# Optimization experiments

Measured on AMD Instinct MI355X. Metric: run time of the kernel, lower is better.

Reference implementation:

```python
import jax, jax.numpy as jnp
import numpy as np
import math

HIDDEN = 2048
NUM_HEADS = 16
NUM_KV_HEADS = 4
HEAD_DIM = 128
GROUPS = NUM_HEADS // NUM_KV_HEADS
BATCH = 1
SEQ = 4096
THETA = 10000.0


def _rope(x):
    # x: [B, h, S, D], interleaved-pair rotation as in the torch module
    seq = x.shape[2]
    freqs = 1.0 / (THETA ** (jnp.arange(0, HEAD_DIM, 2, dtype=jnp.float32) / HEAD_DIM))  # [D/2]
    angles = jnp.arange(seq, dtype=jnp.float32)[:, None] * freqs[None, :]  # [S, D/2]
    cos = jnp.cos(angles)[None, None]  # [1,1,S,D/2]
    sin = jnp.sin(angles)[None, None]
    x1 = x[..., 0::2]
    x2 = x[..., 1::2]
    # stack along new last axis then flatten -> interleaved layout
    rot = jnp.stack([x1 * cos - x2 * sin, x1 * sin + x2 * cos], axis=-1)
    return rot.reshape(x.shape)


def setup_inputs() -> dict:
    key = jax.random.key(0)
    kx, kq, kk, kv, ko = jax.random.split(key, 5)
    scale = 0.02
    x = jax.random.normal(kx, (BATCH, SEQ, HIDDEN), dtype=jnp.float32)
    Wq = jax.random.normal(kq, (NUM_HEADS * HEAD_DIM, HIDDEN), dtype=jnp.float32) * scale
    Wk = jax.random.normal(kk, (NUM_KV_HEADS * HEAD_DIM, HIDDEN), dtype=jnp.float32) * scale
    Wv = jax.random.normal(kv, (NUM_KV_HEADS * HEAD_DIM, HIDDEN), dtype=jnp.float32) * scale
    Wo = jax.random.normal(ko, (HIDDEN, NUM_HEADS * HEAD_DIM), dtype=jnp.float32) * scale
    return {"x": x, "Wq": Wq, "Wk": Wk, "Wv": Wv, "Wo": Wo}


def reference(x, Wq, Wk, Wv, Wo):
    B, S, _ = x.shape
    q = (x @ Wq.T).reshape(B, S, NUM_HEADS, HEAD_DIM).transpose(0, 2, 1, 3)      # [B,16,S,D]
    k = (x @ Wk.T).reshape(B, S, NUM_KV_HEADS, HEAD_DIM).transpose(0, 2, 1, 3)   # [B,4,S,D]
    v = (x @ Wv.T).reshape(B, S, NUM_KV_HEADS, HEAD_DIM).transpose(0, 2, 1, 3)
    q = _rope(q)
    k = _rope(k)
    # GQA: repeat_interleave KV heads across the group dim
    k = jnp.repeat(k, GROUPS, axis=1)  # [B,16,S,D]
    v = jnp.repeat(v, GROUPS, axis=1)
    scale = 1.0 / math.sqrt(HEAD_DIM)
    scores = jnp.einsum("bhqd,bhkd->bhqk", q, k) * scale  # [B,16,S,S]
    causal = jnp.triu(jnp.ones((S, S), dtype=bool), k=1)
    scores = jnp.where(causal[None, None], jnp.float32(-jnp.inf), scores)
    attn = jax.nn.softmax(scores, axis=-1)
    out = jnp.einsum("bhqk,bhkd->bhqd", attn, v)           # [B,16,S,D]
    out = out.transpose(0, 2, 1, 3).reshape(B, S, NUM_HEADS * HEAD_DIM)
    return out @ Wo.T
```

## Files before the change

### kernel.cpp

```cpp
#include <hip/hip_runtime.h>
#include <hip/hip_bf16.h>

typedef unsigned short u16;
typedef unsigned int u32;
typedef short short8 __attribute__((ext_vector_type(8)));
typedef unsigned short ushort4v __attribute__((ext_vector_type(4)));
typedef float f32x4 __attribute__((ext_vector_type(4)));
typedef float f32x16 __attribute__((ext_vector_type(16)));
typedef u32 u32x4 __attribute__((ext_vector_type(4)));

#define SEQN 4096
#define HID 2048
#define NH 16
#define NKV 4
#define HD 128
#define QDIM 2048
#define KVD 512
#define QKVS 3072

static __device__ __forceinline__ float bf2f(u16 u){
  unsigned x = ((unsigned)u) << 16; float f; __builtin_memcpy(&f, &x, 4); return f;
}
static __device__ __forceinline__ u16 f2bf(float f){
  unsigned x; __builtin_memcpy(&x, &f, 4);
  x += 0x7fffu + ((x >> 16) & 1u);
  return (u16)(x >> 16);
}
static __device__ __forceinline__ u16 f2bfc(float f){
  unsigned x; __builtin_memcpy(&x, &f, 4);
  return (u16)((x + 0x8000u) >> 16);
}
static __device__ __forceinline__ u32 pkr(float a, float b){
  u32 ab, bb; __builtin_memcpy(&ab, &a, 4); __builtin_memcpy(&bb, &b, 4);
  return ((ab + 0x8000u) >> 16) | ((bb + 0x8000u) & 0xffff0000u);
}

#define G1 (SEQN*HID/4)
#define G2 (QDIM*HID/4)
#define G3 (KVD*HID/4)
#define G4 (KVD*HID/4)
#define G5 (HID*QDIM/4)
__global__ __launch_bounds__(256) void cvt5_kernel(const float* __restrict__ x,  const float* __restrict__ Wq,
                                                   const float* __restrict__ Wk, const float* __restrict__ Wv,
                                                   const float* __restrict__ Wo, u16* __restrict__ xb,
                                                   u16* __restrict__ Wqkvb, u16* __restrict__ Wob){
  int g = blockIdx.x * 256 + threadIdx.x;
  const float* src; u16* dst; int off;
  if (g < G1)                { src = x;  dst = xb;    off = g; }
  else if (g < G1+G2)        { src = Wq; dst = Wqkvb; off = g - G1; }
  else if (g < G1+G2+G3)     { src = Wk; dst = Wqkvb + (size_t)QDIM*HID;        off = g - (G1+G2); }
  else if (g < G1+G2+G3+G4)  { src = Wv; dst = Wqkvb + (size_t)(QDIM+KVD)*HID;  off = g - (G1+G2+G3); }
  else if (g < G1+G2+G3+G4+G5){ src = Wo; dst = Wob;  off = g - (G1+G2+G3+G4); }
  else return;
  f32x4 v = ((const f32x4*)src)[off];
  ushort4v o;
  o.x = f2bf(v.x); o.y = f2bf(v.y); o.z = f2bf(v.z); o.w = f2bf(v.w);
  ((ushort4v*)dst)[off] = o;
}

#define ROPE_BLKS (SEQN * (NH + NKV) * 16 / 256)
__global__ __launch_bounds__(256) void prep_kernel(u16* __restrict__ QKVb, u16* __restrict__ VTg){
  __shared__ u16 T[64][72];
  const int bid = blockIdx.x;
  const int tid = threadIdx.x;
  if (bid < ROPE_BLKS){
    int idx = bid * 256 + tid;
    int i8 = idx & 15;
    int rest = idx >> 4;
    int h = rest % (NH + NKV);
    int s = rest / (NH + NKV);
    int col = (h < NH) ? h * HD : QDIM + (h - NH) * HD;
    u16* p = QKVb + (size_t)s * QKVS + col + i8 * 8;
    short8 v = *(const short8*)p;
    short8 o;
#pragma unroll
    for (int j = 0; j < 4; j++){
      int i = i8 * 4 + j;
      float freq = expf(-0.14391156831212788f * (float)i);
      float ang = (float)s * freq;
      float c = cosf(ang), sn = sinf(ang);
      float x1 = bf2f((u16)v[2*j]), x2 = bf2f((u16)v[2*j+1]);
      o[2*j]   = (short)f2bfc(x1 * c - x2 * sn);
      o[2*j+1] = (short)f2bfc(x1 * sn + x2 * c);
    }
    *(short8*)p = o;
  } else {
    const int b2 = bid - ROPE_BLKS;
    const int s0 = (b2 & 63) * 64;
    const int c0 = (b2 >> 6) * 64;
    const int sl = tid & 63, ch = tid >> 6;
    const u16* src = QKVb + QDIM + KVD + (size_t)(s0 + sl) * QKVS + c0 + ch * 16;
    *(short8*)&T[sl][ch * 16]     = *(const short8*)(src);
    *(short8*)&T[sl][ch * 16 + 8] = *(const short8*)(src + 8);
    __syncthreads();
#pragma unroll
    for (int it = 0; it < 16; it++){
      int c = it * 4 + ch;
      VTg[(size_t)(c0 + c) * SEQN + s0 + sl] = T[sl][c];
    }
  }
}

static __device__ __forceinline__ void gload16(const void* g, void* l){
  __builtin_amdgcn_global_load_lds((const __attribute__((address_space(1))) void*)g,
                                   (__attribute__((address_space(3))) void*)l, 16, 0, 0);
}

template<int F32OUT>
__global__ __launch_bounds__(256) void gemm_kernel(const u16* __restrict__ A, const u16* __restrict__ B,
                                                   void* __restrict__ Cout, int M, int N, int Kd, int ldc){
  __shared__ alignas(16) u16 sh[32768];
  const int tid = threadIdx.x;
  const int w = tid >> 6, l = tid & 63;
  const int wr = w >> 1, wc = w & 1;
  const int lc = l & 15, lg = l >> 4;
  const int tm = blockIdx.x * 128, tn = blockIdx.y * 128;

  const u16* src[4];
#pragma unroll
  for (int i = 0; i < 4; i++){
    int blk = w * 4 + i;
    int row = (blk & 7) * 16 + (l >> 2);
    int cs  = (l & 3) ^ (row & 3);
    src[i] = (blk < 8) ? (A + (size_t)(tm + row) * Kd + cs * 8)
                       : (B + (size_t)(tn + row) * Kd + cs * 8);
  }

  auto issueStage = [&](int slot, int t){
    char* base = (char*)sh + slot * 16384;
    int k0 = t * 32;
#pragma unroll
    for (int i = 0; i < 4; i++)
      gload16(src[i] + k0, base + (w * 4 + i) * 1024);
  };

  f32x4 acc[4][4] = {};
  const int T = Kd / 32;

  issueStage(0, 0);
  issueStage(1, 1);

  for (int t = 0; t < T; t++){
    if (t + 2 < T) issueStage((t + 2) & 3, t + 2);
    if (t + 2 < T)      asm volatile("s_waitcnt vmcnt(8)" ::: "memory");
    else if (t + 1 < T) asm volatile("s_waitcnt vmcnt(4)" ::: "memory");
    else                asm volatile("s_waitcnt vmcnt(0)" ::: "memory");
    __builtin_amdgcn_s_barrier();
    __builtin_amdgcn_sched_barrier(0);

    const char* base = (const char*)sh + (t & 3) * 16384;
    short8 a[4], b[4];
#pragma unroll
    for (int mi = 0; mi < 4; mi++){
      int row = wr * 64 + mi * 16 + lc;
      a[mi] = *(const short8*)(base + row * 64 + ((lg ^ (row & 3)) * 16));
    }
#pragma unroll
    for (int ni = 0; ni < 4; ni++){
      int row = wc * 64 + ni * 16 + lc;
      b[ni] = *(const short8*)(base + 8192 + row * 64 + ((lg ^ (row & 3)) * 16));
    }
#pragma unroll
    for (int mi = 0; mi < 4; mi++)
#pragma unroll
      for (int ni = 0; ni < 4; ni++)
        acc[mi][ni] = __builtin_amdgcn_mfma_f32_16x16x32_bf16(a[mi], b[ni], acc[mi][ni], 0, 0, 0);
  }

  if (F32OUT){
#pragma unroll
    for (int mi = 0; mi < 4; mi++)
#pragma unroll
      for (int ni = 0; ni < 4; ni++)
#pragma unroll
        for (int r = 0; r < 4; r++){
          int row = tm + wr*64 + mi*16 + lg*4 + r;
          int col = tn + wc*64 + ni*16 + lc;
          ((float*)Cout)[(size_t)row * ldc + col] = acc[mi][ni][r];
        }
  } else {
    __syncthreads();
    u16* Ew = sh + w * 1168;
#pragma unroll
    for (int mi = 0; mi < 4; mi++){
#pragma unroll
      for (int ni = 0; ni < 4; ni++)
#pragma unroll
        for (int r = 0; r < 4; r++)
          Ew[(lg * 4 + r) * 73 + ni * 16 + lc] = f2bfc(acc[mi][ni][r]);
#pragma unroll
      for (int pass = 0; pass < 2; pass++){
        int row = pass * 8 + (l >> 3);
        short8 v;
#pragma unroll
        for (int j = 0; j < 8; j++) v[j] = (short)Ew[row * 73 + (l & 7) * 8 + j];
        *(short8*)((u16*)Cout + (size_t)(tm + wr*64 + mi*16 + row) * ldc + tn + wc*64 + (l & 7) * 8) = v;
      }
    }
  }
}

__global__ __launch_bounds__(256, 2) void attn_kernel(const u16* __restrict__ Qg, const u16* __restrict__ Kgb,
                                                      const u16* __restrict__ VTg, u16* __restrict__ Aout,
                                                      u16* __restrict__ PO, float* __restrict__ mP,
                                                      float* __restrict__ LP){
  __shared__ alignas(16) char pool[65536];

  const int pr  = blockIdx.x;
  const int h   = blockIdx.y;
  const int s   = blockIdx.z;
  const int kvh = h >> 2;
  const int tid = threadIdx.x;
  const int w = tid >> 6, l = tid & 63;
  const int q5 = l & 31;
  const int hi = l >> 5;
  const int hi4 = hi * 4;
  const float csc = 0.12751743f;

  const u16* Ksrc[4];
  const u16* Vsrc[4];
#pragma unroll
  for (int i = 0; i < 4; i++){
    int blk = w * 4 + i;
    int row = blk * 4 + (l >> 4);
    int cg  = (l & 15) ^ (row & 15);
    Ksrc[i] = Kgb + (size_t)row * QKVS + kvh * HD + cg * 8;
    int d   = blk * 8 + (l >> 3);
    int cv  = (l & 7) ^ (d & 7);
    Vsrc[i] = VTg + (size_t)(kvh * 128 + d) * SEQN + cv * 8;
  }

  auto issueTile = [&](int b, int kv0){
    char* Ksb = pool + b * 32768;
    char* VTb = Ksb + 16384;
#pragma unroll
    for (int i = 0; i < 4; i++)
      gload16(Ksrc[i] + (size_t)kv0 * QKVS, Ksb + (w * 4 + i) * 1024);
#pragma unroll
    for (int i = 0; i < 4; i++)
      gload16(Vsrc[i] + kv0, VTb + (w * 4 + i) * 1024);
  };

  const int qlo = pr, qhi = 31 - pr;
  int nseg, sq[2], st0[2], st1[2], smode[2];
  if (s == 0){
    nseg = 2;
    sq[0] = qlo; st0[0] = 0;           st1[0] = 2 * pr + 2;   smode[0] = 0;
    sq[1] = qhi; st0[1] = 0;           st1[1] = 31 - 2 * pr;  smode[1] = 1;
  } else {
    nseg = 1;
    sq[0] = qhi; st0[0] = 31 - 2 * pr; st1[0] = 64 - 2 * pr;  smode[0] = 2;
  }

  for (int sg = 0; sg < nseg; sg++){
    const int qt = sq[sg], t0 = st0[sg], t1 = st1[sg], mode = smode[sg];
    const int qbase = qt * 128 + w * 32;
    const int qa    = qbase + q5;

    short8 qf[8];
    {
      const u16* qp = Qg + (size_t)(qbase + q5) * QKVS + h * HD + hi * 8;
#pragma unroll
      for (int k0 = 0; k0 < 8; k0++) qf[k0] = *(const short8*)(qp + k0 * 16);
    }

    f32x16 Ov[4] = {};
    float Lrow = 0.f;
    float ms = -1e30f;

    auto computeTile = [&](int b, int kv0){
      if (kv0 > qbase + 31) return;
      char* Ksb = pool + b * 32768;
      char* VTb = Ksb + 16384;
      f32x16 Sv[2] = {};
#pragma unroll
      for (int k0 = 0; k0 < 8; k0++){
#pragma unroll
        for (int nb = 0; nb < 2; nb++){
          int kvr = nb * 32 + q5;
          short8 kf = *(const short8*)(Ksb + kvr * 256 + (((k0 * 2 + hi) ^ (kvr & 15)) << 4));
          Sv[nb] = __builtin_amdgcn_mfma_f32_32x32x16_bf16(kf, qf[k0], Sv[nb], 0, 0, 0);
        }
      }
      if (kv0 + 63 > qbase){
#pragma unroll
        for (int nb = 0; nb < 2; nb++)
#pragma unroll
          for (int r = 0; r < 16; r++){
            int kva = kv0 + nb * 32 + (r & 3) + 8 * (r >> 2) + hi4;
            if (kva > qa) Sv[nb][r] = -1e30f;
          }
      }
      float tm = fmaxf(Sv[0][0], Sv[0][1]);
#pragma unroll
      for (int nb = 0; nb < 2; nb++)
#pragma unroll
        for (int r = (nb == 0 ? 2 : 0); r < 16; r += 2)
          tm = fmaxf(tm, fmaxf(Sv[nb][r], Sv[nb][r + 1]));
      tm = fmaxf(tm, __shfl_xor(tm, 32));
      float tms = tm * csc;
      if (!__all(tms - ms <= 8.f)){
        float nms = fmaxf(ms, tms);
        float al = __builtin_amdgcn_exp2f(ms - nms);
        ms = nms;
        Lrow *= al;
#pragma unroll
        for (int nb = 0; nb < 4; nb++)
#pragma unroll
          for (int r = 0; r < 16; r++) Ov[nb][r] *= al;
      }
      float ts0 = 0.f, ts1 = 0.f;
#pragma unroll
      for (int nb = 0; nb < 2; nb++)
#pragma unroll
        for (int r = 0; r < 16; r += 2){
          float p0 = __builtin_amdgcn_exp2f(__builtin_fmaf(Sv[nb][r],     csc, -ms));
          float p1 = __builtin_amdgcn_exp2f(__builtin_fmaf(Sv[nb][r + 1], csc, -ms));
          Sv[nb][r] = p0; Sv[nb][r + 1] = p1;
          ts0 += p0; ts1 += p1;
        }
      float ts = ts0 + ts1;
      ts += __shfl_xor(ts, 32);
      Lrow += ts;
#pragma unroll
      for (int kc = 0; kc < 4; kc++){
        const int nb = kc >> 1, rb = (kc & 1) * 8;
        u32 Aw = pkr(Sv[nb][rb + 0], Sv[nb][rb + 1]);
        u32 Bw = pkr(Sv[nb][rb + 2], Sv[nb][rb + 3]);
        u32 Cw = pkr(Sv[nb][rb + 4], Sv[nb][rb + 5]);
        u32 Dw = pkr(Sv[nb][rb + 6], Sv[nb][rb + 7]);
        u32 sAw = __shfl_xor(Aw, 32);
        u32 sBw = __shfl_xor(Bw, 32);
        u32 sCw = __shfl_xor(Cw, 32);
        u32 sDw = __shfl_xor(Dw, 32);
        u32 w0 = hi ? sCw : Aw;
        u32 w1 = hi ? sDw : Bw;
        u32 w2 = hi ? Cw : sAw;
        u32 w3 = hi ? Dw : sBw;
        u32x4 pw4 = {w0, w1, w2, w3};
        short8 pf = *(short8*)&pw4;
#pragma unroll
        for (int nbd = 0; nbd < 4; nbd++){
          int drow = nbd * 32 + q5;
          short8 vf = *(const short8*)(VTb + drow * 128 + (((kc * 2 + hi) ^ (drow & 7)) << 4));
          Ov[nbd] = __builtin_amdgcn_mfma_f32_32x32x16_bf16(vf, pf, Ov[nbd], 0, 0, 0);
        }
      }
    };

    __syncthreads();
    issueTile(0, t0 * 64);
    __syncthreads();
    int cur = 0;
    for (int t = t0; t < t1; t++){
      if (t + 1 < t1) issueTile(cur ^ 1, (t + 1) * 64);
      computeTile(cur, t * 64);
      __syncthreads();
      cur ^= 1;
    }

    u16* Ew = (u16*)(pool + w * 8704);
    float rl = (mode == 0) ? (1.f / Lrow) : 1.f;
#pragma unroll
    for (int nbd = 0; nbd < 4; nbd++)
#pragma unroll
      for (int r = 0; r < 16; r += 2){
        int d = nbd * 32 + (r & 3) + 8 * (r >> 2) + hi4;
        u32 wpk = pkr(Ov[nbd][r] * rl, Ov[nbd][r + 1] * rl);
        *(u32*)((char*)Ew + q5 * 272 + d * 2) = wpk;
      }
    if (mode == 0){
#pragma unroll
      for (int pass = 0; pass < 8; pass++){
        int q2 = pass * 4 + (l >> 4);
        short8 ov = *(const short8*)((char*)Ew + q2 * 272 + (l & 15) * 16);
        *(short8*)(Aout + (size_t)(qbase + q2) * QDIM + h * HD + (l & 15) * 8) = ov;
      }
    } else {
      const int p = mode - 1;
      u16* dstb = PO + ((size_t)((p * 16 + pr) * NH + h) * 128) * 128;
#pragma unroll
      for (int pass = 0; pass < 8; pass++){
        int q2 = pass * 4 + (l >> 4);
        short8 ov = *(const short8*)((char*)Ew + q2 * 272 + (l & 15) * 16);
        *(short8*)(dstb + (size_t)(w * 32 + q2) * 128 + (l & 15) * 8) = ov;
      }
      if (hi == 0){
        int idx = ((p * 16 + pr) * NH + h) * 128 + w * 32 + q5;
        mP[idx] = ms;
        LP[idx] = Lrow;
      }
    }
  }
}

__global__ __launch_bounds__(256) void combine_kernel(const u16* __restrict__ PO, const float* __restrict__ mP,
                                                      const float* __restrict__ LP, u16* __restrict__ Aout){
  const int pr = blockIdx.x;
  const int h  = blockIdx.y;
  const int tid = threadIdx.x;
  const int r  = tid >> 1;
  const int dh = (tid & 1) * 64;
  const int qhi = 31 - pr;
  const int idx0 = ((0 * 16 + pr) * NH + h) * 128 + r;
  const int idx1 = ((1 * 16 + pr) * NH + h) * 128 + r;
  float m0 = mP[idx0], m1 = mP[idx1];
  float L0 = LP[idx0], L1 = LP[idx1];
  float M = fmaxf(m0, m1);
  float a0 = __builtin_amdgcn_exp2f(m0 - M);
  float a1 = __builtin_amdgcn_exp2f(m1 - M);
  float rl = 1.f / (L0 * a0 + L1 * a1);
  const u16* o0 = PO + (size_t)idx0 * 128 + dh;
  const u16* o1 = PO + (size_t)idx1 * 128 + dh;
  u16* dst = Aout + (size_t)(qhi * 128 + r) * QDIM + h * HD + dh;
#pragma unroll
  for (int ch = 0; ch < 8; ch++){
    short8 v0 = *(const short8*)(o0 + ch * 8);
    short8 v1 = *(const short8*)(o1 + ch * 8);
    u32x4 ow;
#pragma unroll
    for (int j = 0; j < 4; j++){
      float e0 = (bf2f((u16)v0[2*j])   * a0 + bf2f((u16)v1[2*j])   * a1) * rl;
      float e1 = (bf2f((u16)v0[2*j+1]) * a0 + bf2f((u16)v1[2*j+1]) * a1) * rl;
      ow[j] = pkr(e0, e1);
    }
    *(u32x4*)(dst + ch * 8) = ow;
  }
}

extern "C" void kernel_launch(void* const* d_in, const int* in_sizes, int n_in,
                              void* d_out, int out_size, void* d_ws, size_t ws_size,
                              hipStream_t stream){
  const float* x  = (const float*)d_in[0];
  const float* Wq = (const float*)d_in[1];
  const float* Wk = (const float*)d_in[2];
  const float* Wv = (const float*)d_in[3];
  const float* Wo = (const float*)d_in[4];

  char* p = (char*)d_ws;
  u16* xb    = (u16*)p; p += (size_t)SEQN * HID * 2;
  u16* Wqkvb = (u16*)p; p += (size_t)QKVS * HID * 2;
  u16* Wob   = (u16*)p; p += (size_t)HID * QDIM * 2;
  u16* QKVb  = (u16*)p; p += (size_t)SEQN * QKVS * 2;
  u16* Ab    = (u16*)p; p += (size_t)SEQN * QDIM * 2;
  u16* VTg   = (u16*)p; p += (size_t)SEQN * KVD * 2;
  u16* PO    = (u16*)p; p += (size_t)2 * 16 * NH * 128 * 128 * 2;
  float* mP  = (float*)p; p += (size_t)2 * 16 * NH * 128 * 4;
  float* LP  = (float*)p; p += (size_t)2 * 16 * NH * 128 * 4;

  const int totg = G1 + G2 + G3 + G4 + G5;
  cvt5_kernel<<<(totg + 255) / 256, 256, 0, stream>>>(x, Wq, Wk, Wv, Wo, xb, Wqkvb, Wob);

  gemm_kernel<0><<<dim3(SEQN/128, QKVS/128), 256, 0, stream>>>(xb, Wqkvb, QKVb, SEQN, QKVS, HID, QKVS);

  prep_kernel<<<ROPE_BLKS + (SEQN/64) * (KVD/64), 256, 0, stream>>>(QKVb, VTg);

  attn_kernel<<<dim3(16, NH, 2), 256, 0, stream>>>(QKVb, QKVb + QDIM, VTg, Ab, PO, mP, LP);
  combine_kernel<<<dim3(16, NH), 256, 0, stream>>>(PO, mP, LP, Ab);

  gemm_kernel<1><<<dim3(SEQN/128, HID/128), 256, 0, stream>>>(Ab, Wob, d_out, SEQN, HID, QDIM, HID);
}
```

Before: 238.2 us.

## Deepen GEMM pipeline, swizzle block order for XCD locality, raise MFMA priority

The GEMM now uses a five-slot LDS ring with three stages in flight instead of two, adjusting the vmcnt waits to match. It also remaps workgroup IDs so that consecutive tiles land on the same XCD for L2 reuse. The attention kernel remaps its block index so heads sharing a KV head are grouped per XCD, and it wraps its MFMA loops in s_setprio to favour matrix issue. The extra GEMM stage raises LDS use per block, which may lower occupancy. The GEMM swizzle assumes the workgroup count divides evenly by 8.

Result: slower. 245.3 us (+3.0%).

```diff
diff --git a/kernel.cpp b/kernel.cpp
--- a/kernel.cpp
+++ b/kernel.cpp
@@ -109,12 +109,18 @@
 template<int F32OUT>
 __global__ __launch_bounds__(256) void gemm_kernel(const u16* __restrict__ A, const u16* __restrict__ B,
                                                    void* __restrict__ Cout, int M, int N, int Kd, int ldc){
-  __shared__ alignas(16) u16 sh[32768];
+  __shared__ alignas(16) u16 sh[40960];
   const int tid = threadIdx.x;
   const int w = tid >> 6, l = tid & 63;
   const int wr = w >> 1, wc = w & 1;
   const int lc = l & 15, lg = l >> 4;
-  const int tm = blockIdx.x * 128, tn = blockIdx.y * 128;
+
+  const int nbx = gridDim.x;
+  const int nwg = nbx * gridDim.y;
+  const int fid = blockIdx.x + nbx * blockIdx.y;
+  const int cpx = nwg >> 3;
+  const int swz = (fid & 7) * cpx + (fid >> 3);
+  const int tm = (swz % nbx) * 128, tn = (swz / nbx) * 128;
 
   const u16* src[4];
 #pragma unroll
@@ -138,17 +144,21 @@
   const int T = Kd / 32;
 
   issueStage(0, 0);
-  issueStage(1, 1);
-
+  if (1 < T) issueStage(1, 1);
+  if (2 < T) issueStage(2, 2);
+
+  int sw = 3, sr = 0;
   for (int t = 0; t < T; t++){
-    if (t + 2 < T) issueStage((t + 2) & 3, t + 2);
-    if (t + 2 < T)      asm volatile("s_waitcnt vmcnt(8)" ::: "memory");
-    else if (t + 1 < T) asm volatile("s_waitcnt vmcnt(4)" ::: "memory");
-    else                asm volatile("s_waitcnt vmcnt(0)" ::: "memory");
+    if (t + 3 < T){ issueStage(sw, t + 3); if (++sw == 5) sw = 0; }
+    if (t + 3 < T)      asm volatile("s_waitcnt vmcnt(12)" ::: "memory");
+    else if (t + 2 < T) asm volatile("s_waitcnt vmcnt(8)"  ::: "memory");
+    else if (t + 1 < T) asm volatile("s_waitcnt vmcnt(4)"  ::: "memory");
+    else                asm volatile("s_waitcnt vmcnt(0)"  ::: "memory");
     __builtin_amdgcn_s_barrier();
     __builtin_amdgcn_sched_barrier(0);
 
-    const char* base = (const char*)sh + (t & 3) * 16384;
+    const char* base = (const char*)sh + sr * 16384;
+    if (++sr == 5) sr = 0;
     short8 a[4], b[4];
 #pragma unroll
     for (int mi = 0; mi < 4; mi++){
@@ -206,9 +216,12 @@
                                                       float* __restrict__ LP){
   __shared__ alignas(16) char pool[65536];
 
-  const int pr  = blockIdx.x;
-  const int h   = blockIdx.y;
-  const int s   = blockIdx.z;
+  const int fid = blockIdx.x + 16 * (blockIdx.y + NH * blockIdx.z);
+  const int c8  = fid & 7;
+  const int idx = ((c8 & 1) << 6) | (fid >> 3);
+  const int pr  = (idx >> 2) & 15;
+  const int s   = idx >> 6;
+  const int h   = 4 * (c8 >> 1) + (idx & 3);
   const int kvh = h >> 2;
   const int tid = threadIdx.x;
   const int w = tid >> 6, l = tid & 63;
@@ -273,6 +286,7 @@
       char* Ksb = pool + b * 32768;
       char* VTb = Ksb + 16384;
       f32x16 Sv[2] = {};
+      __builtin_amdgcn_s_setprio(1);
 #pragma unroll
       for (int k0 = 0; k0 < 8; k0++){
 #pragma unroll
@@ -282,6 +296,7 @@
           Sv[nb] = __builtin_amdgcn_mfma_f32_32x32x16_bf16(kf, qf[k0], Sv[nb], 0, 0, 0);
         }
       }
+      __builtin_amdgcn_s_setprio(0);
       if (kv0 + 63 > qbase){
 #pragma unroll
         for (int nb = 0; nb < 2; nb++)
@@ -339,12 +354,14 @@
         u32 w3 = hi ? Dw : sBw;
         u32x4 pw4 = {w0, w1, w2, w3};
         short8 pf = *(short8*)&pw4;
+        __builtin_amdgcn_s_setprio(1);
 #pragma unroll
         for (int nbd = 0; nbd < 4; nbd++){
           int drow = nbd * 32 + q5;
           short8 vf = *(const short8*)(VTb + drow * 128 + (((kc * 2 + hi) ^ (drow & 7)) << 4));
           Ov[nbd] = __builtin_amdgcn_mfma_f32_32x32x16_bf16(vf, pf, Ov[nbd], 0, 0, 0);
         }
+        __builtin_amdgcn_s_setprio(0);
       }
     };
 
@@ -386,9 +403,9 @@
         *(short8*)(dstb + (size_t)(w * 32 + q2) * 128 + (l & 15) * 8) = ov;
       }
       if (hi == 0){
-        int idx = ((p * 16 + pr) * NH + h) * 128 + w * 32 + q5;
-        mP[idx] = ms;
-        LP[idx] = Lrow;
+        int idx2 = ((p * 16 + pr) * NH + h) * 128 + w * 32 + q5;
+        mP[idx2] = ms;
+        LP[idx2] = Lrow;
       }
     }
   }
```
